# Kernel optimization log

Hardware: AMD Instinct MI355X
Metric: run time of the kernel (lower is better)

## Reference

```python
import jax, jax.numpy as jnp
import numpy as np

B, L, E = 4, 2048, 1024
H, DQ, DV = 8, 128, 128
SCALE = 1.0 / np.sqrt(DQ).astype(np.float32)


def setup_inputs() -> dict:
    key = jax.random.key(0)
    ks = jax.random.split(key, 6)
    return {
        "qInputs": jax.random.normal(ks[0], (B, L, E), dtype=jnp.float32),
        "kvInputs": jax.random.normal(ks[1], (B, L, E), dtype=jnp.float32),
        "mask": jnp.zeros((B, H, L, L), dtype=jnp.bool_),
        "W_Q": jax.random.normal(ks[2], (E, H * DQ), dtype=jnp.float32) * 0.02,
        "W_K": jax.random.normal(ks[3], (E, H * DQ), dtype=jnp.float32) * 0.02,
        "W_V": jax.random.normal(ks[4], (E, H * DV), dtype=jnp.float32) * 0.02,
        "W_fc": jax.random.normal(ks[5], (H * DV, E), dtype=jnp.float32) * 0.02,
    }


def reference(qInputs, kvInputs, mask, W_Q, W_K, W_V, W_fc):
    b, lq, _ = qInputs.shape
    lk = kvInputs.shape[1]
    # Projections -> [B, H, L, D]
    Q = (qInputs @ W_Q).reshape(b, lq, H, DQ).transpose(0, 2, 1, 3)
    K = (kvInputs @ W_K).reshape(b, lk, H, DQ).transpose(0, 2, 1, 3)
    V = (kvInputs @ W_V).reshape(b, lk, H, DV).transpose(0, 2, 1, 3)
    # Scaled dot-product with additive mask fill of -1e9
    scores = jnp.einsum("bhqd,bhkd->bhqk", Q, K) * SCALE
    scores = jnp.where(mask, jnp.float32(-1e9), scores)
    attn = jax.nn.softmax(scores, axis=-1)
    ctx = jnp.einsum("bhqk,bhkd->bhqd", attn, V)
    ctx = ctx.transpose(0, 2, 1, 3).reshape(b, lq, H * DV)
    return ctx @ W_fc
```

## Files before the change

### kernel.cpp

```cpp
#include <hip/hip_runtime.h>
#include <stdint.h>

#define LQ 2048
#define EDIM 1024
#define HN 8
#define DH 128
#define BATCH 4
#define SCALE_LOG2E 0.12753785051263942f

typedef short bf16x8 __attribute__((ext_vector_type(8)));
typedef float f32x4 __attribute__((ext_vector_type(4)));
typedef unsigned short u16;
typedef unsigned short u16x4 __attribute__((ext_vector_type(4)));

__device__ __forceinline__ u16 f2bf(float f) {
  union { float f; uint32_t u; } c; c.f = f;
  uint32_t u = c.u;
  return (u16)((u + 0x7fffu + ((u >> 16) & 1u)) >> 16);
}

__device__ __forceinline__ void async16(const void* g, void* l) {
  __builtin_amdgcn_global_load_lds((const __attribute__((address_space(1))) void*)g,
                                   (__attribute__((address_space(3))) void*)l, 16, 0, 0);
}

__global__ __launch_bounds__(256) void cvt_kernel(const float* __restrict__ xq,
                                                  const float* __restrict__ xkv,
                                                  u16* __restrict__ oq, u16* __restrict__ okv) {
  const float* in = blockIdx.y ? xkv : xq;
  u16* out = blockIdx.y ? okv : oq;
  size_t i = (size_t)blockIdx.x * 256 + threadIdx.x;
  float4 v = ((const float4*)in)[i];
  u16x4 o;
  o.x = f2bf(v.x); o.y = f2bf(v.y); o.z = f2bf(v.z); o.w = f2bf(v.w);
  ((u16x4*)out)[i] = o;
}

__global__ __launch_bounds__(256) void transpose_cvt(const float* __restrict__ w0, const float* __restrict__ w1,
                                                     const float* __restrict__ w2, const float* __restrict__ w3,
                                                     u16* __restrict__ o0, u16* __restrict__ o1,
                                                     u16* __restrict__ o2, u16* __restrict__ o3) {
  const float* in; u16* out;
  switch (blockIdx.z) {
    case 0: in = w0; out = o0; break;
    case 1: in = w1; out = o1; break;
    case 2: in = w2; out = o2; break;
    default: in = w3; out = o3; break;
  }
  __shared__ float tile[32][33];
  int tx = threadIdx.x, ty = threadIdx.y;
  int x0 = blockIdx.x * 32;
  int y0 = blockIdx.y * 32;
#pragma unroll
  for (int j = 0; j < 32; j += 8)
    tile[ty + j][tx] = in[(size_t)(y0 + ty + j) * EDIM + x0 + tx];
  __syncthreads();
#pragma unroll
  for (int j = 0; j < 32; j += 8)
    out[(size_t)(x0 + ty + j) * EDIM + (y0 + tx)] = f2bf(tile[tx][ty + j]);
}

__global__ __launch_bounds__(256) void mask_scan(const unsigned char* __restrict__ mask,
                                                 unsigned char* __restrict__ flags) {
  const int qt = blockIdx.x >> 4;
  const int kt = blockIdx.x & 15;
  const int h = blockIdx.y;
  const int b = blockIdx.z;
  const int t = threadIdx.x;
  const int r = t >> 1;
  const size_t base = ((size_t)(b * HN + h) * LQ + qt * 128 + r) * LQ + kt * 128 + (t & 1) * 64;
  const uint4* p = (const uint4*)(mask + base);
  uint4 a = p[0], c = p[1], d = p[2], e = p[3];
  uint32_t any = a.x | a.y | a.z | a.w | c.x | c.y | c.z | c.w |
                 d.x | d.y | d.z | d.w | e.x | e.y | e.z | e.w;
  __shared__ int wany[4];
  int wa = __any(any != 0);
  if ((t & 63) == 0) wany[t >> 6] = wa;
  __syncthreads();
  if (t == 0)
    flags[(size_t)(b * HN + h) * 256 + blockIdx.x] =
        (unsigned char)(wany[0] | wany[1] | wany[2] | wany[3]);
}

template <int MODE>
__global__ __launch_bounds__(256) void gemm_bt(const u16* __restrict__ A, const u16* __restrict__ Bt,
                                               void* __restrict__ C) {
  __shared__ __align__(16) u16 As[128 * 32];
  __shared__ __align__(16) u16 Bs[128 * 32];
  const int tid = threadIdx.x;
  const int l = tid & 63;
  const int w = tid >> 6;
  const int m0 = blockIdx.x * 128;
  const int n0 = blockIdx.y * 128;
  const int wm = (w >> 1) * 64;
  const int wn = (w & 1) * 64;
  const int lrow = l >> 2;
  const int lk8 = (l & 3) * 8;
  const int fm = l & 15;
  const int fk = (l >> 4) * 8;
  f32x4 acc[4][4] = {};
  for (int k0 = 0; k0 < EDIM; k0 += 32) {
    __syncthreads();
#pragma unroll
    for (int ii = 0; ii < 2; ++ii) {
      int i = w * 2 + ii;
      async16(A + (size_t)(m0 + i * 16 + lrow) * EDIM + k0 + lk8, &As[i * 512 + l * 8]);
      async16(Bt + (size_t)(n0 + i * 16 + lrow) * EDIM + k0 + lk8, &Bs[i * 512 + l * 8]);
    }
    __syncthreads();
    bf16x8 a[4], b[4];
#pragma unroll
    for (int i = 0; i < 4; ++i) a[i] = *(const bf16x8*)&As[(wm + i * 16 + fm) * 32 + fk];
#pragma unroll
    for (int j = 0; j < 4; ++j) b[j] = *(const bf16x8*)&Bs[(wn + j * 16 + fm) * 32 + fk];
#pragma unroll
    for (int i = 0; i < 4; ++i)
#pragma unroll
      for (int j = 0; j < 4; ++j)
        acc[i][j] = __builtin_amdgcn_mfma_f32_16x16x32_bf16(a[i], b[j], acc[i][j], 0, 0, 0);
  }
  const int rr = (l >> 4) * 4;
#pragma unroll
  for (int i = 0; i < 4; ++i)
#pragma unroll
    for (int j = 0; j < 4; ++j)
#pragma unroll
      for (int r = 0; r < 4; ++r) {
        int gm = m0 + wm + i * 16 + rr + r;
        int gn = n0 + wn + j * 16 + fm;
        float v = acc[i][j][r];
        if (MODE == 0) {
          ((u16*)C)[(size_t)gm * EDIM + gn] = f2bf(v);
        } else if (MODE == 1) {
          ((u16*)C)[((size_t)(gn >> 11) * 1024 + gm) * 2048 + (gn & 2047)] = f2bf(v);
        } else {
          ((float*)C)[(size_t)gm * EDIM + gn] = v;
        }
      }
}

__global__ __launch_bounds__(256, 2) void attn_kernel(const u16* __restrict__ Qb, const u16* __restrict__ Kb,
                                                      const u16* __restrict__ Vt,
                                                      const unsigned char* __restrict__ mask,
                                                      const unsigned char* __restrict__ flags,
                                                      u16* __restrict__ ctx) {
  __shared__ __align__(16) u16 KV[128 * 128];
  __shared__ __align__(16) u16 P[128 * 136];
  const int tid = threadIdx.x;
  const int l = tid & 63;
  const int w = tid >> 6;
  const int qt = blockIdx.x;
  const int h = blockIdx.y;
  const int b = blockIdx.z;
  const int fm = l & 15;
  const int q4 = l >> 4;
  const int fk = q4 * 8;
  const int swz = fm & 7;
  const int qbase = qt * 128 + w * 32;

  const unsigned char* tileFlags = flags + (size_t)(b * HN + h) * 256 + qt * 16;

  bf16x8 qf[2][4];
#pragma unroll
  for (int mt = 0; mt < 2; ++mt)
#pragma unroll
    for (int ks = 0; ks < 4; ++ks)
      qf[mt][ks] = *(const bf16x8*)(Qb + (size_t)(b * LQ + qbase + mt * 16 + fm) * EDIM + h * DH + ks * 32 + fk);

  f32x4 o[2][8] = {};
  float lsum[2][4] = {};

  const size_t mbase = (size_t)(b * HN + h) * (size_t)LQ * LQ;

  for (int kt = 0; kt < 16; ++kt) {
    __syncthreads();
#pragma unroll
    for (int ii = 0; ii < 8; ++ii) {
      int rloc = w * 32 + ii * 4 + q4;
      int cs = fm ^ (rloc & 7);
      async16(Kb + (size_t)(b * LQ + kt * 128 + rloc) * EDIM + h * DH + cs * 8,
              &KV[(w * 32 + ii * 4) * 128 + l * 8]);
    }
    __syncthreads();

    f32x4 s[2][8] = {};
#pragma unroll
    for (int ks = 0; ks < 4; ++ks) {
      const int koff = ((ks * 4 + q4) ^ swz) * 8;
#pragma unroll
      for (int nt = 0; nt < 8; ++nt) {
        bf16x8 kf = *(const bf16x8*)&KV[(nt * 16 + fm) * 128 + koff];
        s[0][nt] = __builtin_amdgcn_mfma_f32_16x16x32_bf16(qf[0][ks], kf, s[0][nt], 0, 0, 0);
        s[1][nt] = __builtin_amdgcn_mfma_f32_16x16x32_bf16(qf[1][ks], kf, s[1][nt], 0, 0, 0);
      }
    }
    __syncthreads();

#pragma unroll
    for (int ii = 0; ii < 8; ++ii) {
      int dloc = w * 32 + ii * 4 + q4;
      int cs = fm ^ (dloc & 7);
      async16(Vt + ((size_t)(b * HN + h) * DH + dloc) * LQ + kt * 128 + cs * 8,
              &KV[(w * 32 + ii * 4) * 128 + l * 8]);
    }

    const int hasMask = tileFlags[kt];
#pragma unroll
    for (int mt = 0; mt < 2; ++mt)
#pragma unroll
      for (int r = 0; r < 4; ++r) {
        float sum = 0.f;
        if (hasMask) {
          const int qr = qbase + mt * 16 + q4 * 4 + r;
          const unsigned char* mrow = mask + mbase + (size_t)qr * LQ + kt * 128 + fm;
#pragma unroll
          for (int nt = 0; nt < 8; ++nt) {
            float e = mrow[nt * 16] ? 0.f : exp2f(s[mt][nt][r] * SCALE_LOG2E);
            s[mt][nt][r] = e;
            sum += e;
          }
        } else {
#pragma unroll
          for (int nt = 0; nt < 8; ++nt) {
            float e = exp2f(s[mt][nt][r] * SCALE_LOG2E);
            s[mt][nt][r] = e;
            sum += e;
          }
        }
#pragma unroll
        for (int off = 1; off < 16; off <<= 1) sum += __shfl_xor(sum, off);
        lsum[mt][r] += sum;
      }
#pragma unroll
    for (int mt = 0; mt < 2; ++mt)
#pragma unroll
      for (int r = 0; r < 4; ++r)
#pragma unroll
        for (int nt = 0; nt < 8; ++nt)
          P[(w * 32 + mt * 16 + q4 * 4 + r) * 136 + nt * 16 + fm] = f2bf(s[mt][nt][r]);
    __syncthreads();

#pragma unroll
    for (int ns = 0; ns < 4; ++ns) {
      const int voff = ((ns * 4 + q4) ^ swz) * 8;
      bf16x8 pf0 = *(const bf16x8*)&P[(w * 32 + fm) * 136 + ns * 32 + fk];
      bf16x8 pf1 = *(const bf16x8*)&P[(w * 32 + 16 + fm) * 136 + ns * 32 + fk];
#pragma unroll
      for (int dt = 0; dt < 8; ++dt) {
        bf16x8 vf = *(const bf16x8*)&KV[(dt * 16 + fm) * 128 + voff];
        o[0][dt] = __builtin_amdgcn_mfma_f32_16x16x32_bf16(pf0, vf, o[0][dt], 0, 0, 0);
        o[1][dt] = __builtin_amdgcn_mfma_f32_16x16x32_bf16(pf1, vf, o[1][dt], 0, 0, 0);
      }
    }
  }
#pragma unroll
  for (int mt = 0; mt < 2; ++mt)
#pragma unroll
    for (int r = 0; r < 4; ++r) {
      float inv = 1.f / lsum[mt][r];
      int gq = b * LQ + qbase + mt * 16 + q4 * 4 + r;
#pragma unroll
      for (int dt = 0; dt < 8; ++dt)
        ctx[(size_t)gq * EDIM + h * DH + dt * 16 + fm] = f2bf(o[mt][dt][r] * inv);
    }
}

extern "C" void kernel_launch(void* const* d_in, const int* in_sizes, int n_in,
                              void* d_out, int out_size, void* d_ws, size_t ws_size,
                              hipStream_t stream) {
  const float* qIn = (const float*)d_in[0];
  const float* kvIn = (const float*)d_in[1];
  const unsigned char* mask = (const unsigned char*)d_in[2];
  const float* W_Q = (const float*)d_in[3];
  const float* W_K = (const float*)d_in[4];
  const float* W_V = (const float*)d_in[5];
  const float* W_fc = (const float*)d_in[6];
  float* out = (float*)d_out;

  uint8_t* ws = (uint8_t*)d_ws;
  const size_t MB = 1u << 20;
  u16* xq   = (u16*)(ws);
  u16* xkv  = (u16*)(ws + 16 * MB);
  u16* WqT  = (u16*)(ws + 32 * MB);
  u16* WkT  = (u16*)(ws + 34 * MB);
  u16* WvT  = (u16*)(ws + 36 * MB);
  u16* WfcT = (u16*)(ws + 38 * MB);
  u16* Qb   = (u16*)(ws + 40 * MB);
  u16* Kb   = (u16*)(ws + 56 * MB);
  u16* Vt   = (u16*)(ws + 72 * MB);
  u16* ctx  = (u16*)(ws + 88 * MB);
  unsigned char* flags = (unsigned char*)(ws + 104 * MB);

  cvt_kernel<<<dim3(8192, 2), 256, 0, stream>>>(qIn, kvIn, xq, xkv);
  transpose_cvt<<<dim3(32, 32, 4), dim3(32, 8), 0, stream>>>(W_Q, W_K, W_V, W_fc, WqT, WkT, WvT, WfcT);
  mask_scan<<<dim3(256, 8, 4), 256, 0, stream>>>(mask, flags);
  gemm_bt<0><<<dim3(64, 8), 256, 0, stream>>>(xq, WqT, Qb);
  gemm_bt<0><<<dim3(64, 8), 256, 0, stream>>>(xkv, WkT, Kb);
  gemm_bt<1><<<dim3(8, 64), 256, 0, stream>>>(WvT, xkv, Vt);
  attn_kernel<<<dim3(16, 8, 4), 256, 0, stream>>>(Qb, Kb, Vt, mask, flags, ctx);
  gemm_bt<2><<<dim3(64, 8), 256, 0, stream>>>(ctx, WfcT, out);
}
```

Measured before the change: 920.8 us.

## Merge prep kernels, batch QKV GEMMs, widen GEMM K-tile with swizzled LDS

Folds the input conversion, weight transpose and mask scan into one prep launch, and runs the Q, K and V projections as a single 3-slice grid. The shared GEMM core now loads a 64-wide K tile per step with an XOR swizzle on the LDS columns, to cut bank conflicts and halve the number of barrier pairs. The aim is less launch overhead and better occupancy for the small projection GEMMs. In exchange, LDS use per block doubles and the prep kernel's branches diverge at block level.

```diff
diff --git a/kernel.cpp b/kernel.cpp
--- a/kernel.cpp
+++ b/kernel.cpp
@@ -24,119 +24,143 @@
                                    (__attribute__((address_space(3))) void*)l, 16, 0, 0);
 }
 
-__global__ __launch_bounds__(256) void cvt_kernel(const float* __restrict__ xq,
-                                                  const float* __restrict__ xkv,
-                                                  u16* __restrict__ oq, u16* __restrict__ okv) {
-  const float* in = blockIdx.y ? xkv : xq;
-  u16* out = blockIdx.y ? okv : oq;
-  size_t i = (size_t)blockIdx.x * 256 + threadIdx.x;
-  float4 v = ((const float4*)in)[i];
-  u16x4 o;
-  o.x = f2bf(v.x); o.y = f2bf(v.y); o.z = f2bf(v.z); o.w = f2bf(v.w);
-  ((u16x4*)out)[i] = o;
-}
-
-__global__ __launch_bounds__(256) void transpose_cvt(const float* __restrict__ w0, const float* __restrict__ w1,
-                                                     const float* __restrict__ w2, const float* __restrict__ w3,
-                                                     u16* __restrict__ o0, u16* __restrict__ o1,
-                                                     u16* __restrict__ o2, u16* __restrict__ o3) {
-  const float* in; u16* out;
-  switch (blockIdx.z) {
-    case 0: in = w0; out = o0; break;
-    case 1: in = w1; out = o1; break;
-    case 2: in = w2; out = o2; break;
-    default: in = w3; out = o3; break;
+__global__ __launch_bounds__(256) void prep_kernel(const float* __restrict__ qIn, const float* __restrict__ kvIn,
+                                                   const float* __restrict__ w0, const float* __restrict__ w1,
+                                                   const float* __restrict__ w2, const float* __restrict__ w3,
+                                                   const unsigned char* __restrict__ mask,
+                                                   u16* __restrict__ oq, u16* __restrict__ okv,
+                                                   u16* __restrict__ o0, u16* __restrict__ o1,
+                                                   u16* __restrict__ o2, u16* __restrict__ o3,
+                                                   unsigned char* __restrict__ flags) {
+  __shared__ float tile[32][33];
+  __shared__ int wany[4];
+  const int bid = blockIdx.x;
+  const int t = threadIdx.x;
+  if (bid < 16384) {
+    const float* in = (bid >= 8192) ? kvIn : qIn;
+    u16* out = (bid >= 8192) ? okv : oq;
+    size_t i = (size_t)(bid & 8191) * 256 + t;
+    float4 v = ((const float4*)in)[i];
+    u16x4 o;
+    o.x = f2bf(v.x); o.y = f2bf(v.y); o.z = f2bf(v.z); o.w = f2bf(v.w);
+    ((u16x4*)out)[i] = o;
+  } else if (bid < 20480) {
+    const int idx = bid - 16384;
+    const int z = idx >> 10;
+    const int rem = idx & 1023;
+    const float* in; u16* out;
+    switch (z) {
+      case 0: in = w0; out = o0; break;
+      case 1: in = w1; out = o1; break;
+      case 2: in = w2; out = o2; break;
+      default: in = w3; out = o3; break;
+    }
+    const int tx = t & 31, ty = t >> 5;
+    const int x0 = (rem & 31) * 32;
+    const int y0 = (rem >> 5) * 32;
+#pragma unroll
+    for (int j = 0; j < 32; j += 8)
+      tile[ty + j][tx] = in[(size_t)(y0 + ty + j) * EDIM + x0 + tx];
+    __syncthreads();
+#pragma unroll
+    for (int j = 0; j < 32; j += 8)
+      out[(size_t)(x0 + ty + j) * EDIM + (y0 + tx)] = f2bf(tile[tx][ty + j]);
+  } else {
+    const int idx = bid - 20480;
+    const int bh = idx >> 8;
+    const int tile16 = idx & 255;
+    const int qt = tile16 >> 4, kt = tile16 & 15;
+    const int r = t >> 1;
+    const size_t base = ((size_t)bh * LQ + qt * 128 + r) * LQ + kt * 128 + (t & 1) * 64;
+    const uint4* p = (const uint4*)(mask + base);
+    uint4 a = p[0], c = p[1], d = p[2], e = p[3];
+    uint32_t any = a.x | a.y | a.z | a.w | c.x | c.y | c.z | c.w |
+                   d.x | d.y | d.z | d.w | e.x | e.y | e.z | e.w;
+    int wa = __any(any != 0);
+    if ((t & 63) == 0) wany[t >> 6] = wa;
+    __syncthreads();
+    if (t == 0)
+      flags[(size_t)bh * 256 + tile16] = (unsigned char)(wany[0] | wany[1] | wany[2] | wany[3]);
   }
-  __shared__ float tile[32][33];
-  int tx = threadIdx.x, ty = threadIdx.y;
-  int x0 = blockIdx.x * 32;
-  int y0 = blockIdx.y * 32;
-#pragma unroll
-  for (int j = 0; j < 32; j += 8)
-    tile[ty + j][tx] = in[(size_t)(y0 + ty + j) * EDIM + x0 + tx];
-  __syncthreads();
-#pragma unroll
-  for (int j = 0; j < 32; j += 8)
-    out[(size_t)(x0 + ty + j) * EDIM + (y0 + tx)] = f2bf(tile[tx][ty + j]);
-}
-
-__global__ __launch_bounds__(256) void mask_scan(const unsigned char* __restrict__ mask,
-                                                 unsigned char* __restrict__ flags) {
-  const int qt = blockIdx.x >> 4;
-  const int kt = blockIdx.x & 15;
-  const int h = blockIdx.y;
-  const int b = blockIdx.z;
-  const int t = threadIdx.x;
-  const int r = t >> 1;
-  const size_t base = ((size_t)(b * HN + h) * LQ + qt * 128 + r) * LQ + kt * 128 + (t & 1) * 64;
-  const uint4* p = (const uint4*)(mask + base);
-  uint4 a = p[0], c = p[1], d = p[2], e = p[3];
-  uint32_t any = a.x | a.y | a.z | a.w | c.x | c.y | c.z | c.w |
-                 d.x | d.y | d.z | d.w | e.x | e.y | e.z | e.w;
-  __shared__ int wany[4];
-  int wa = __any(any != 0);
-  if ((t & 63) == 0) wany[t >> 6] = wa;
-  __syncthreads();
-  if (t == 0)
-    flags[(size_t)(b * HN + h) * 256 + blockIdx.x] =
-        (unsigned char)(wany[0] | wany[1] | wany[2] | wany[3]);
-}
-
-template <int MODE>
-__global__ __launch_bounds__(256) void gemm_bt(const u16* __restrict__ A, const u16* __restrict__ Bt,
-                                               void* __restrict__ C) {
-  __shared__ __align__(16) u16 As[128 * 32];
-  __shared__ __align__(16) u16 Bs[128 * 32];
-  const int tid = threadIdx.x;
-  const int l = tid & 63;
-  const int w = tid >> 6;
-  const int m0 = blockIdx.x * 128;
-  const int n0 = blockIdx.y * 128;
-  const int wm = (w >> 1) * 64;
-  const int wn = (w & 1) * 64;
-  const int lrow = l >> 2;
-  const int lk8 = (l & 3) * 8;
-  const int fm = l & 15;
-  const int fk = (l >> 4) * 8;
-  f32x4 acc[4][4] = {};
-  for (int k0 = 0; k0 < EDIM; k0 += 32) {
-    __syncthreads();
-#pragma unroll
-    for (int ii = 0; ii < 2; ++ii) {
-      int i = w * 2 + ii;
-      async16(A + (size_t)(m0 + i * 16 + lrow) * EDIM + k0 + lk8, &As[i * 512 + l * 8]);
-      async16(Bt + (size_t)(n0 + i * 16 + lrow) * EDIM + k0 + lk8, &Bs[i * 512 + l * 8]);
-    }
-    __syncthreads();
-    bf16x8 a[4], b[4];
-#pragma unroll
-    for (int i = 0; i < 4; ++i) a[i] = *(const bf16x8*)&As[(wm + i * 16 + fm) * 32 + fk];
-#pragma unroll
-    for (int j = 0; j < 4; ++j) b[j] = *(const bf16x8*)&Bs[(wn + j * 16 + fm) * 32 + fk];
+}
+
+struct GemmCore {
+  template <typename EpiF>
+  static __device__ __forceinline__ void run(const u16* __restrict__ A, const u16* __restrict__ Bt,
+                                             int m0, int n0, u16* As, u16* Bs, EpiF epi) {
+    const int tid = threadIdx.x;
+    const int l = tid & 63;
+    const int w = tid >> 6;
+    const int wm = (w >> 1) * 64;
+    const int wn = (w & 1) * 64;
+    const int fm = l & 15;
+    const int q4 = l >> 4;
+    const int f7 = fm & 7;
+    f32x4 acc[4][4] = {};
+    for (int k0 = 0; k0 < EDIM; k0 += 64) {
+      __syncthreads();
+#pragma unroll
+      for (int ii = 0; ii < 4; ++ii) {
+        const int rloc = w * 32 + ii * 8 + (l >> 3);
+        const int cs = (l & 7) ^ (rloc & 7);
+        async16(A + (size_t)(m0 + rloc) * EDIM + k0 + cs * 8, &As[(w * 32 + ii * 8) * 64 + l * 8]);
+        async16(Bt + (size_t)(n0 + rloc) * EDIM + k0 + cs * 8, &Bs[(w * 32 + ii * 8) * 64 + l * 8]);
+      }
+      __syncthreads();
+#pragma unroll
+      for (int ks = 0; ks < 2; ++ks) {
+        const int coff = ((ks * 4 + q4) ^ f7) * 8;
+        bf16x8 a[4], b[4];
+#pragma unroll
+        for (int i = 0; i < 4; ++i) a[i] = *(const bf16x8*)&As[(wm + i * 16 + fm) * 64 + coff];
+#pragma unroll
+        for (int j = 0; j < 4; ++j) b[j] = *(const bf16x8*)&Bs[(wn + j * 16 + fm) * 64 + coff];
+#pragma unroll
+        for (int i = 0; i < 4; ++i)
+#pragma unroll
+          for (int j = 0; j < 4; ++j)
+            acc[i][j] = __builtin_amdgcn_mfma_f32_16x16x32_bf16(a[i], b[j], acc[i][j], 0, 0, 0);
+      }
+    }
+    const int rr = q4 * 4;
 #pragma unroll
     for (int i = 0; i < 4; ++i)
 #pragma unroll
       for (int j = 0; j < 4; ++j)
-        acc[i][j] = __builtin_amdgcn_mfma_f32_16x16x32_bf16(a[i], b[j], acc[i][j], 0, 0, 0);
+#pragma unroll
+        for (int r = 0; r < 4; ++r)
+          epi(m0 + wm + i * 16 + rr + r, n0 + wn + j * 16 + fm, acc[i][j][r]);
   }
-  const int rr = (l >> 4) * 4;
-#pragma unroll
-  for (int i = 0; i < 4; ++i)
-#pragma unroll
-    for (int j = 0; j < 4; ++j)
-#pragma unroll
-      for (int r = 0; r < 4; ++r) {
-        int gm = m0 + wm + i * 16 + rr + r;
-        int gn = n0 + wn + j * 16 + fm;
-        float v = acc[i][j][r];
-        if (MODE == 0) {
-          ((u16*)C)[(size_t)gm * EDIM + gn] = f2bf(v);
-        } else if (MODE == 1) {
-          ((u16*)C)[((size_t)(gn >> 11) * 1024 + gm) * 2048 + (gn & 2047)] = f2bf(v);
-        } else {
-          ((float*)C)[(size_t)gm * EDIM + gn] = v;
-        }
-      }
+};
+
+__global__ __launch_bounds__(256) void qkv_gemm(const u16* __restrict__ xq, const u16* __restrict__ xkv,
+                                                const u16* __restrict__ WqT, const u16* __restrict__ WkT,
+                                                const u16* __restrict__ WvT,
+                                                u16* __restrict__ Qb, u16* __restrict__ Kb,
+                                                u16* __restrict__ Vt) {
+  __shared__ __align__(16) u16 As[128 * 64];
+  __shared__ __align__(16) u16 Bs[128 * 64];
+  const int z = blockIdx.z;
+  if (z == 0) {
+    GemmCore::run(xq, WqT, blockIdx.x * 128, blockIdx.y * 128, As, Bs,
+                  [&](int gm, int gn, float v) { Qb[(size_t)gm * EDIM + gn] = f2bf(v); });
+  } else if (z == 1) {
+    GemmCore::run(xkv, WkT, blockIdx.x * 128, blockIdx.y * 128, As, Bs,
+                  [&](int gm, int gn, float v) { Kb[(size_t)gm * EDIM + gn] = f2bf(v); });
+  } else {
+    GemmCore::run(WvT, xkv, blockIdx.y * 128, blockIdx.x * 128, As, Bs,
+                  [&](int gm, int gn, float v) {
+                    Vt[((size_t)(gn >> 11) * 1024 + gm) * 2048 + (gn & 2047)] = f2bf(v);
+                  });
+  }
+}
+
+__global__ __launch_bounds__(256) void out_gemm(const u16* __restrict__ ctx, const u16* __restrict__ WfcT,
+                                                float* __restrict__ out) {
+  __shared__ __align__(16) u16 As[128 * 64];
+  __shared__ __align__(16) u16 Bs[128 * 64];
+  GemmCore::run(ctx, WfcT, blockIdx.x * 128, blockIdx.y * 128, As, Bs,
+                [&](int gm, int gn, float v) { out[(size_t)gm * EDIM + gn] = v; });
 }
 
 __global__ __launch_bounds__(256, 2) void attn_kernel(const u16* __restrict__ Qb, const u16* __restrict__ Kb,
@@ -291,12 +315,9 @@
   u16* ctx  = (u16*)(ws + 88 * MB);
   unsigned char* flags = (unsigned char*)(ws + 104 * MB);
 
-  cvt_kernel<<<dim3(8192, 2), 256, 0, stream>>>(qIn, kvIn, xq, xkv);
-  transpose_cvt<<<dim3(32, 32, 4), dim3(32, 8), 0, stream>>>(W_Q, W_K, W_V, W_fc, WqT, WkT, WvT, WfcT);
-  mask_scan<<<dim3(256, 8, 4), 256, 0, stream>>>(mask, flags);
-  gemm_bt<0><<<dim3(64, 8), 256, 0, stream>>>(xq, WqT, Qb);
-  gemm_bt<0><<<dim3(64, 8), 256, 0, stream>>>(xkv, WkT, Kb);
-  gemm_bt<1><<<dim3(8, 64), 256, 0, stream>>>(WvT, xkv, Vt);
+  prep_kernel<<<28672, 256, 0, stream>>>(qIn, kvIn, W_Q, W_K, W_V, W_fc, mask,
+                                         xq, xkv, WqT, WkT, WvT, WfcT, flags);
+  qkv_gemm<<<dim3(64, 8, 3), 256, 0, stream>>>(xq, xkv, WqT, WkT, WvT, Qb, Kb, Vt);
   attn_kernel<<<dim3(16, 8, 4), 256, 0, stream>>>(Qb, Kb, Vt, mask, flags, ctx);
-  gemm_bt<2><<<dim3(64, 8), 256, 0, stream>>>(ctx, WfcT, out);
-}
+  out_gemm<<<dim3(64, 8), 256, 0, stream>>>(ctx, WfcT, out);
+}
```

After: 895.9 us. -2.7%, faster.
